# Optimization experiments

Hardware: AMD Instinct MI355X
Metric: run time of the kernel (lower is better)

Reference implementation:

```python
import jax, jax.numpy as jnp
import numpy as np

C_IN = 1024
N_HEADS = 16
C_HEAD = C_IN // N_HEADS  # 64
ROPE_BASE = 10000.0


def setup_inputs() -> dict:
    key = jax.random.key(0)
    ks = jax.random.split(key, 7)
    B, S = 2, 2048
    q = jax.random.normal(ks[0], (B, S, C_IN), dtype=jnp.float32)
    k = jax.random.normal(ks[1], (B, S, C_IN), dtype=jnp.float32)
    v = jax.random.normal(ks[2], (B, S, C_IN), dtype=jnp.float32)
    # nn.Linear weights [out, in], y = x @ W.T (no bias)
    sc = 1.0 / np.sqrt(C_IN)
    Wq = jax.random.uniform(ks[3], (C_IN, C_IN), jnp.float32, -sc, sc)
    Wk = jax.random.uniform(ks[4], (C_IN, C_IN), jnp.float32, -sc, sc)
    Wv = jax.random.uniform(ks[5], (C_IN, C_IN), jnp.float32, -sc, sc)
    Wo = jax.random.uniform(ks[6], (C_IN, C_IN), jnp.float32, -sc, sc)
    return {"q": q, "k": k, "v": v, "Wq": Wq, "Wk": Wk, "Wv": Wv, "Wo": Wo}


def _rope_tables(S, dtype):
    inv_freq = 1.0 / (ROPE_BASE ** (jnp.arange(0, C_HEAD, 2, dtype=jnp.float32) / C_HEAD))
    t = jnp.arange(S, dtype=jnp.float32)
    freqs = jnp.einsum('i,j->ij', t, inv_freq)          # [S, C_HEAD/2]
    emb = jnp.concatenate([freqs, freqs], axis=-1)      # [S, C_HEAD]
    cos = jnp.cos(emb)[None, None, :, :].astype(dtype)  # [1,1,S,D]
    sin = jnp.sin(emb)[None, None, :, :].astype(dtype)
    return cos, sin


def _rotate_half(x):
    x1, x2 = jnp.split(x, 2, axis=-1)
    return jnp.concatenate([-x2, x1], axis=-1)


def reference(q, k, v, Wq, Wk, Wv, Wo):
    B, S, _ = q.shape
    # QKV projections, reshape to [B, H, S, D]
    def proj(x, W):
        return (x @ W.T).reshape(B, -1, N_HEADS, C_HEAD).transpose(0, 2, 1, 3)
    qh, kh, vh = proj(q, Wq), proj(k, Wk), proj(v, Wv)
    # rotary embedding
    cos, sin = _rope_tables(S, qh.dtype)
    qh = qh * cos + _rotate_half(qh) * sin
    kh = kh * cos + _rotate_half(kh) * sin
    # scaled dot-product attention (no mask, dropout p=0)
    scale = 1.0 / np.sqrt(C_HEAD)
    scores = jnp.einsum('bhqd,bhkd->bhqk', qh, kh) * scale
    attn = jax.nn.softmax(scores, axis=-1)              # [B,H,S,S]
    out = jnp.einsum('bhqk,bhkd->bhqd', attn, vh)
    out = out.transpose(0, 2, 1, 3).reshape(B, S, N_HEADS * C_HEAD)
    out = out @ Wo.T
    return out, attn
```

## Files before the change

### kernel.cpp

```cpp
#include <hip/hip_runtime.h>
#include <cmath>

typedef __bf16 bhalf;
typedef __bf16 bf16x4 __attribute__((ext_vector_type(4)));
typedef __bf16 bf16x8 __attribute__((ext_vector_type(8)));
typedef float f32x4 __attribute__((ext_vector_type(4)));

#define MFMA16(a, b, c) __builtin_amdgcn_mfma_f32_16x16x32_bf16(a, b, c, 0, 0, 0)

namespace {
constexpr int Bn = 2, Sn = 2048, Cn = 1024, Hn = 16, Dn = 64;
constexpr int Zn = Bn * Hn;
constexpr int Mn = Bn * Sn;
}

__device__ __forceinline__ void cvt_hilo8(const float4& v0, const float4& v1,
                                          bf16x8& hi, bf16x8& lo) {
  float f[8] = {v0.x, v0.y, v0.z, v0.w, v1.x, v1.y, v1.z, v1.w};
#pragma unroll
  for (int i = 0; i < 8; ++i) {
    bhalf h = (bhalf)f[i];
    hi[i] = h;
    lo[i] = (bhalf)(f[i] - (float)h);
  }
}

template <int MODE, bool A_BF16>
__global__ __launch_bounds__(256) void proj_mfma(
    const void* __restrict__ Av, const void* __restrict__ AvLo,
    const float* __restrict__ W, float* __restrict__ out_f32,
    bhalf* __restrict__ dst_hi, bhalf* __restrict__ dst_lo) {
  __shared__ bhalf BsH[64][40];
  __shared__ bhalf BsL[64][40];
  const int tid = threadIdx.x;
  const int lane = tid & 63, w = tid >> 6;
  const int l15 = lane & 15, lg = lane >> 4;
  const int nB = blockIdx.x << 6, mB = blockIdx.y << 6;
  const int row = mB + w * 16 + l15;
  f32x4 acc[4] = {};

  const int sr = tid >> 2, sc = (tid & 3) << 3;
  for (int k0 = 0; k0 < Cn; k0 += 32) {
    {
      const float* wp = W + (size_t)(nB + sr) * Cn + k0 + sc;
      float4 w0 = *(const float4*)wp;
      float4 w1 = *(const float4*)(wp + 4);
      bf16x8 h, l;
      cvt_hilo8(w0, w1, h, l);
      *(bf16x8*)&BsH[sr][sc] = h;
      *(bf16x8*)&BsL[sr][sc] = l;
    }
    __syncthreads();
    bf16x8 aH, aL;
    if constexpr (A_BF16) {
      aH = *(const bf16x8*)((const bhalf*)Av + (size_t)row * Cn + k0 + lg * 8);
      aL = *(const bf16x8*)((const bhalf*)AvLo + (size_t)row * Cn + k0 + lg * 8);
    } else {
      const float* A = (const float*)Av;
      float4 a0 = *(const float4*)(A + (size_t)row * Cn + k0 + lg * 8);
      float4 a1 = *(const float4*)(A + (size_t)row * Cn + k0 + lg * 8 + 4);
      cvt_hilo8(a0, a1, aH, aL);
    }
#pragma unroll
    for (int j = 0; j < 4; ++j) {
      bf16x8 bH = *(const bf16x8*)&BsH[16 * j + l15][lg * 8];
      bf16x8 bL = *(const bf16x8*)&BsL[16 * j + l15][lg * 8];
      acc[j] = MFMA16(aH, bH, acc[j]);
      acc[j] = MFMA16(aH, bL, acc[j]);
      acc[j] = MFMA16(aL, bH, acc[j]);
    }
    __syncthreads();
  }

  const int mRow = mB + w * 16 + lg * 4;
  if constexpr (MODE == 0) {
#pragma unroll
    for (int j = 0; j < 4; ++j) {
      const int n = nB + 16 * j + l15;
#pragma unroll
      for (int r = 0; r < 4; ++r)
        out_f32[(size_t)(mRow + r) * Cn + n] = acc[j][r];
    }
  } else if constexpr (MODE == 1) {
    const int hh = nB >> 6;
#pragma unroll
    for (int jj = 0; jj < 2; ++jj) {
      const int d1 = 16 * jj + l15;
      const float invf = 1.0f / powf(10000.0f, (float)d1 * (1.0f / 32.0f));
#pragma unroll
      for (int r = 0; r < 4; ++r) {
        const int m = mRow + r;
        const int b = m >> 11, s = m & (Sn - 1);
        float sn, cs;
        sincosf((float)s * invf, &sn, &cs);
        const float y1 = acc[jj][r], y2 = acc[jj + 2][r];
        const float o1 = y1 * cs - y2 * sn;
        const float o2 = y2 * cs + y1 * sn;
        const size_t base = (((size_t)(b * Hn + hh)) * Sn + s) * Dn;
        bhalf h1 = (bhalf)o1, h2 = (bhalf)o2;
        dst_hi[base + d1] = h1;
        dst_lo[base + d1] = (bhalf)(o1 - (float)h1);
        dst_hi[base + d1 + 32] = h2;
        dst_lo[base + d1 + 32] = (bhalf)(o2 - (float)h2);
      }
    }
  } else {
    const int hh = nB >> 6;
#pragma unroll
    for (int j = 0; j < 4; ++j) {
      const int d = 16 * j + l15;
#pragma unroll
      for (int r = 0; r < 4; ++r) {
        const int m = mRow + r;
        const int b = m >> 11, s = m & (Sn - 1);
        dst_hi[(((size_t)(b * Hn + hh)) * Dn + d) * Sn + s] = (bhalf)acc[j][r];
      }
    }
  }
}

__device__ __forceinline__ void load_q(const bhalf* __restrict__ qhH,
                                       const bhalf* __restrict__ qhL,
                                       size_t zrow, int sBt, int l15, int lg,
                                       bf16x8 (&qH)[2][2], bf16x8 (&qL)[2][2]) {
#pragma unroll
  for (int qf = 0; qf < 2; ++qf)
#pragma unroll
    for (int sl = 0; sl < 2; ++sl) {
      const size_t off = (zrow + sBt + qf * 16 + l15) * Dn + sl * 32 + lg * 8;
      qH[qf][sl] = *(const bf16x8*)(qhH + off);
      qL[qf][sl] = *(const bf16x8*)(qhL + off);
    }
}

__global__ __launch_bounds__(256) void attn_fused(
    const bhalf* __restrict__ qhH, const bhalf* __restrict__ qhL,
    const bhalf* __restrict__ khH, const bhalf* __restrict__ khL,
    const bhalf* __restrict__ vt, float* __restrict__ attn,
    bhalf* __restrict__ ctxH, bhalf* __restrict__ ctxL) {
  __shared__ float pt[4][32][36];
  __shared__ float lsum[4][32];
  __shared__ float linv[32];

  const int tid = threadIdx.x, lane = tid & 63, w = tid >> 6;
  const int l15 = lane & 15, lg = lane >> 4;
  const int gx = blockIdx.x;
  const int z = gx & 31;
  const int gq = gx >> 5;
  const int sB0 = gq << 7;
  const int bb = z >> 4, hh = z & 15;
  const size_t zrow = (size_t)z * Sn;
  const size_t kRow = zrow * Dn;
  const int kw = w << 9;

  bf16x8 qHc[2][2], qLc[2][2], qHp[2][2], qLp[2][2];
  load_q(qhH, qhL, zrow, sB0, l15, lg, qHc, qLc);

  float invqB[2] = {0.f, 0.f};
  f32x4 acc[2][4];

#pragma unroll 1
  for (int tau = 0; tau <= 4; ++tau) {
    const bool hasA = (tau < 4), hasB = (tau > 0);
    const int sBb = sB0 + ((tau - 1) << 5);
    float sum0 = 0.f, sum1 = 0.f;
    if (hasB) {
#pragma unroll
      for (int qf = 0; qf < 2; ++qf)
#pragma unroll
        for (int g = 0; g < 4; ++g) acc[qf][g] = f32x4{0.f, 0.f, 0.f, 0.f};
    }

#pragma unroll 1
    for (int cc = 0; cc < 16; ++cc) {
      const int kbc = kw + (cc << 5);
#pragma unroll
      for (int t2 = 0; t2 < 2; ++t2) {
        const int kb = kbc + (t2 << 4);
        const bhalf* kp = khH + kRow + (size_t)(kb + l15) * Dn + lg * 8;
        const bhalf* kq = khL + kRow + (size_t)(kb + l15) * Dn + lg * 8;
        bf16x8 kH0 = *(const bf16x8*)kp, kH1 = *(const bf16x8*)(kp + 32);
        bf16x8 kL0 = *(const bf16x8*)kq, kL1 = *(const bf16x8*)(kq + 32);
        if (hasA) {
#pragma unroll
          for (int qf = 0; qf < 2; ++qf) {
            f32x4 cA = {}, cB = {};
            cA = MFMA16(kH0, qHc[qf][0], cA); cA = MFMA16(kH1, qHc[qf][1], cA);
            cB = MFMA16(kL0, qHc[qf][0], cB); cB = MFMA16(kL1, qHc[qf][1], cB);
            cA = MFMA16(kH0, qLc[qf][0], cA); cA = MFMA16(kH1, qLc[qf][1], cA);
            f32x4 c = cA + cB;
            float s = __expf(c[0] * 0.125f) + __expf(c[1] * 0.125f) +
                      __expf(c[2] * 0.125f) + __expf(c[3] * 0.125f);
            if (qf == 0) sum0 += s; else sum1 += s;
          }
        }
        if (hasB) {
#pragma unroll
          for (int qf = 0; qf < 2; ++qf) {
            f32x4 cA = {}, cB = {};
            cA = MFMA16(kH0, qHp[qf][0], cA); cA = MFMA16(kH1, qHp[qf][1], cA);
            cB = MFMA16(kL0, qHp[qf][0], cB); cB = MFMA16(kL1, qHp[qf][1], cB);
            cA = MFMA16(kH0, qLp[qf][0], cA); cA = MFMA16(kH1, qLp[qf][1], cA);
            f32x4 c = cA + cB;
            f32x4 p;
#pragma unroll
            for (int r = 0; r < 4; ++r)
              p[r] = __expf(c[r] * 0.125f) * invqB[qf];
            *(f32x4*)&pt[w][qf * 16 + l15][(t2 << 4) + (lg << 2)] = p;
          }
        }
      }
      if (hasB) {
        const int srow = lane >> 3, scol = (lane & 7) << 2;
#pragma unroll
        for (int s = 0; s < 4; ++s) {
          const int row = (s << 3) + srow;
          f32x4 vv = *(const f32x4*)&pt[w][row][scol];
          __builtin_nontemporal_store(
              vv, (f32x4*)(attn + (zrow + sBb + row) * Sn + kbc + scol));
        }
#pragma unroll
        for (int qf = 0; qf < 2; ++qf) {
          f32x4 pa = *(const f32x4*)&pt[w][qf * 16 + l15][lg << 3];
          f32x4 pc = *(const f32x4*)&pt[w][qf * 16 + l15][(lg << 3) + 4];
          bf16x8 pbv;
#pragma unroll
          for (int e = 0; e < 4; ++e) {
            pbv[e] = (bhalf)pa[e];
            pbv[4 + e] = (bhalf)pc[e];
          }
#pragma unroll
          for (int g = 0; g < 4; ++g) {
            const bf16x8 va = *(const bf16x8*)(
                vt + ((size_t)z * Dn + g * 16 + l15) * Sn + kbc + lg * 8);
            acc[qf][g] = MFMA16(va, pbv, acc[qf][g]);
          }
        }
      }
    }

    if (hasA) {
      sum0 += __shfl_xor(sum0, 16); sum0 += __shfl_xor(sum0, 32);
      sum1 += __shfl_xor(sum1, 16); sum1 += __shfl_xor(sum1, 32);
      if (lane < 16) {
        lsum[w][l15] = sum0;
        lsum[w][16 + l15] = sum1;
      }
    }
    __syncthreads();
    if (hasA && tid < 32)
      linv[tid] =
          1.0f / (lsum[0][tid] + lsum[1][tid] + lsum[2][tid] + lsum[3][tid]);
    if (hasB) {
      float* fb = (float*)&pt[w][0][0];
      float* fb0 = (float*)&pt[0][0][0];
      float* fb1 = (float*)&pt[1][0][0];
      float* fb2 = (float*)&pt[2][0][0];
      float* fb3 = (float*)&pt[3][0][0];
#pragma unroll
      for (int qf = 0; qf < 2; ++qf) {
#pragma unroll
        for (int g = 0; g < 4; ++g)
#pragma unroll
          for (int r = 0; r < 4; ++r)
            fb[l15 * 72 + g * 16 + lg * 4 + r] = acc[qf][g][r];
        __syncthreads();
        {
          const int qq = tid >> 4, d4 = (tid & 15) << 2;
          f32x4 rs = *(const f32x4*)&fb0[qq * 72 + d4];
          rs += *(const f32x4*)&fb1[qq * 72 + d4];
          rs += *(const f32x4*)&fb2[qq * 72 + d4];
          rs += *(const f32x4*)&fb3[qq * 72 + d4];
          const size_t off =
              ((size_t)bb * Sn + sBb + qf * 16 + qq) * Cn + hh * Dn + d4;
          bf16x4 hv, lv;
#pragma unroll
          for (int e = 0; e < 4; ++e) {
            bhalf h = (bhalf)rs[e];
            hv[e] = h;
            lv[e] = (bhalf)(rs[e] - (float)h);
          }
          *(bf16x4*)(ctxH + off) = hv;
          *(bf16x4*)(ctxL + off) = lv;
        }
        __syncthreads();
      }
    } else {
      __syncthreads();
    }
    if (hasA) {
      invqB[0] = linv[l15];
      invqB[1] = linv[16 + l15];
#pragma unroll
      for (int qf = 0; qf < 2; ++qf)
#pragma unroll
        for (int sl = 0; sl < 2; ++sl) {
          qHp[qf][sl] = qHc[qf][sl];
          qLp[qf][sl] = qLc[qf][sl];
        }
      if (tau < 3)
        load_q(qhH, qhL, zrow, sB0 + ((tau + 1) << 5), l15, lg, qHc, qLc);
    }
  }
}

extern "C" void kernel_launch(void* const* d_in, const int* in_sizes, int n_in,
                              void* d_out, int out_size, void* d_ws, size_t ws_size,
                              hipStream_t stream) {
  const float* q = (const float*)d_in[0];
  const float* k = (const float*)d_in[1];
  const float* v = (const float*)d_in[2];
  const float* Wq = (const float*)d_in[3];
  const float* Wk = (const float*)d_in[4];
  const float* Wv = (const float*)d_in[5];
  const float* Wo = (const float*)d_in[6];

  float* out = (float*)d_out;
  float* attn = out + (size_t)Mn * Cn;
  bhalf* vt = (bhalf*)d_out;

  bhalf* qhH = (bhalf*)d_ws;
  bhalf* qhL = qhH + (size_t)Mn * Cn;
  bhalf* khH = qhL + (size_t)Mn * Cn;
  bhalf* khL = khH + (size_t)Mn * Cn;
  bhalf* ctxH = khL + (size_t)Mn * Cn;
  bhalf* ctxL = ctxH + (size_t)Mn * Cn;

  dim3 gP(Cn / 64, Mn / 64);
  proj_mfma<1, false><<<gP, 256, 0, stream>>>(q, nullptr, Wq, nullptr, qhH, qhL);
  proj_mfma<1, false><<<gP, 256, 0, stream>>>(k, nullptr, Wk, nullptr, khH, khL);
  proj_mfma<2, false><<<gP, 256, 0, stream>>>(v, nullptr, Wv, nullptr, vt, nullptr);

  attn_fused<<<Zn * (Sn / 128), 256, 0, stream>>>(qhH, qhL, khH, khL, vt, attn,
                                                  ctxH, ctxL);

  proj_mfma<0, true><<<gP, 256, 0, stream>>>(ctxH, ctxL, Wo, out, nullptr, nullptr);
}
```

Baseline: 433.9 us.

## Double projection GEMM M-tile and split QK MFMA accumulator chains

```diff
diff --git a/kernel.cpp b/kernel.cpp
--- a/kernel.cpp
+++ b/kernel.cpp
@@ -35,9 +35,9 @@
   const int tid = threadIdx.x;
   const int lane = tid & 63, w = tid >> 6;
   const int l15 = lane & 15, lg = lane >> 4;
-  const int nB = blockIdx.x << 6, mB = blockIdx.y << 6;
-  const int row = mB + w * 16 + l15;
-  f32x4 acc[4] = {};
+  const int nB = blockIdx.x << 6, mB = blockIdx.y << 7;
+  const int row0 = mB + w * 32 + l15;
+  f32x4 acc[2][4] = {};
 
   const int sr = tid >> 2, sc = (tid & 3) << 3;
   for (int k0 = 0; k0 < Cn; k0 += 32) {
@@ -51,69 +51,79 @@
       *(bf16x8*)&BsL[sr][sc] = l;
     }
     __syncthreads();
-    bf16x8 aH, aL;
-    if constexpr (A_BF16) {
-      aH = *(const bf16x8*)((const bhalf*)Av + (size_t)row * Cn + k0 + lg * 8);
-      aL = *(const bf16x8*)((const bhalf*)AvLo + (size_t)row * Cn + k0 + lg * 8);
-    } else {
-      const float* A = (const float*)Av;
-      float4 a0 = *(const float4*)(A + (size_t)row * Cn + k0 + lg * 8);
-      float4 a1 = *(const float4*)(A + (size_t)row * Cn + k0 + lg * 8 + 4);
-      cvt_hilo8(a0, a1, aH, aL);
+    bf16x8 aH[2], aL[2];
+#pragma unroll
+    for (int rg = 0; rg < 2; ++rg) {
+      const size_t ro = (size_t)(row0 + rg * 16) * Cn + k0 + lg * 8;
+      if constexpr (A_BF16) {
+        aH[rg] = *(const bf16x8*)((const bhalf*)Av + ro);
+        aL[rg] = *(const bf16x8*)((const bhalf*)AvLo + ro);
+      } else {
+        const float* A = (const float*)Av;
+        float4 a0 = *(const float4*)(A + ro);
+        float4 a1 = *(const float4*)(A + ro + 4);
+        cvt_hilo8(a0, a1, aH[rg], aL[rg]);
+      }
     }
 #pragma unroll
     for (int j = 0; j < 4; ++j) {
       bf16x8 bH = *(const bf16x8*)&BsH[16 * j + l15][lg * 8];
       bf16x8 bL = *(const bf16x8*)&BsL[16 * j + l15][lg * 8];
-      acc[j] = MFMA16(aH, bH, acc[j]);
-      acc[j] = MFMA16(aH, bL, acc[j]);
-      acc[j] = MFMA16(aL, bH, acc[j]);
+#pragma unroll
+      for (int rg = 0; rg < 2; ++rg) {
+        acc[rg][j] = MFMA16(aH[rg], bH, acc[rg][j]);
+        acc[rg][j] = MFMA16(aH[rg], bL, acc[rg][j]);
+        acc[rg][j] = MFMA16(aL[rg], bH, acc[rg][j]);
+      }
     }
     __syncthreads();
   }
 
-  const int mRow = mB + w * 16 + lg * 4;
-  if constexpr (MODE == 0) {
-#pragma unroll
-    for (int j = 0; j < 4; ++j) {
-      const int n = nB + 16 * j + l15;
-#pragma unroll
-      for (int r = 0; r < 4; ++r)
-        out_f32[(size_t)(mRow + r) * Cn + n] = acc[j][r];
-    }
-  } else if constexpr (MODE == 1) {
-    const int hh = nB >> 6;
-#pragma unroll
-    for (int jj = 0; jj < 2; ++jj) {
-      const int d1 = 16 * jj + l15;
-      const float invf = 1.0f / powf(10000.0f, (float)d1 * (1.0f / 32.0f));
-#pragma unroll
-      for (int r = 0; r < 4; ++r) {
-        const int m = mRow + r;
-        const int b = m >> 11, s = m & (Sn - 1);
-        float sn, cs;
-        sincosf((float)s * invf, &sn, &cs);
-        const float y1 = acc[jj][r], y2 = acc[jj + 2][r];
-        const float o1 = y1 * cs - y2 * sn;
-        const float o2 = y2 * cs + y1 * sn;
-        const size_t base = (((size_t)(b * Hn + hh)) * Sn + s) * Dn;
-        bhalf h1 = (bhalf)o1, h2 = (bhalf)o2;
-        dst_hi[base + d1] = h1;
-        dst_lo[base + d1] = (bhalf)(o1 - (float)h1);
-        dst_hi[base + d1 + 32] = h2;
-        dst_lo[base + d1 + 32] = (bhalf)(o2 - (float)h2);
-      }
-    }
-  } else {
-    const int hh = nB >> 6;
-#pragma unroll
-    for (int j = 0; j < 4; ++j) {
-      const int d = 16 * j + l15;
-#pragma unroll
-      for (int r = 0; r < 4; ++r) {
-        const int m = mRow + r;
-        const int b = m >> 11, s = m & (Sn - 1);
-        dst_hi[(((size_t)(b * Hn + hh)) * Dn + d) * Sn + s] = (bhalf)acc[j][r];
+#pragma unroll
+  for (int rg = 0; rg < 2; ++rg) {
+    const int mRow = mB + w * 32 + rg * 16 + lg * 4;
+    if constexpr (MODE == 0) {
+#pragma unroll
+      for (int j = 0; j < 4; ++j) {
+        const int n = nB + 16 * j + l15;
+#pragma unroll
+        for (int r = 0; r < 4; ++r)
+          out_f32[(size_t)(mRow + r) * Cn + n] = acc[rg][j][r];
+      }
+    } else if constexpr (MODE == 1) {
+      const int hh = nB >> 6;
+#pragma unroll
+      for (int jj = 0; jj < 2; ++jj) {
+        const int d1 = 16 * jj + l15;
+        const float invf = 1.0f / powf(10000.0f, (float)d1 * (1.0f / 32.0f));
+#pragma unroll
+        for (int r = 0; r < 4; ++r) {
+          const int m = mRow + r;
+          const int b = m >> 11, s = m & (Sn - 1);
+          float sn, cs;
+          sincosf((float)s * invf, &sn, &cs);
+          const float y1 = acc[rg][jj][r], y2 = acc[rg][jj + 2][r];
+          const float o1 = y1 * cs - y2 * sn;
+          const float o2 = y2 * cs + y1 * sn;
+          const size_t base = (((size_t)(b * Hn + hh)) * Sn + s) * Dn;
+          bhalf h1 = (bhalf)o1, h2 = (bhalf)o2;
+          dst_hi[base + d1] = h1;
+          dst_lo[base + d1] = (bhalf)(o1 - (float)h1);
+          dst_hi[base + d1 + 32] = h2;
+          dst_lo[base + d1 + 32] = (bhalf)(o2 - (float)h2);
+        }
+      }
+    } else {
+      const int hh = nB >> 6;
+#pragma unroll
+      for (int j = 0; j < 4; ++j) {
+        const int d = 16 * j + l15;
+#pragma unroll
+        for (int r = 0; r < 4; ++r) {
+          const int m = mRow + r;
+          const int b = m >> 11, s = m & (Sn - 1);
+          dst_hi[(((size_t)(b * Hn + hh)) * Dn + d) * Sn + s] = (bhalf)acc[rg][j][r];
+        }
       }
     }
   }
@@ -184,11 +194,11 @@
         if (hasA) {
 #pragma unroll
           for (int qf = 0; qf < 2; ++qf) {
-            f32x4 cA = {}, cB = {};
+            f32x4 cA = {}, cB = {}, cC = {};
             cA = MFMA16(kH0, qHc[qf][0], cA); cA = MFMA16(kH1, qHc[qf][1], cA);
             cB = MFMA16(kL0, qHc[qf][0], cB); cB = MFMA16(kL1, qHc[qf][1], cB);
-            cA = MFMA16(kH0, qLc[qf][0], cA); cA = MFMA16(kH1, qLc[qf][1], cA);
-            f32x4 c = cA + cB;
+            cC = MFMA16(kH0, qLc[qf][0], cC); cC = MFMA16(kH1, qLc[qf][1], cC);
+            f32x4 c = (cA + cB) + cC;
             float s = __expf(c[0] * 0.125f) + __expf(c[1] * 0.125f) +
                       __expf(c[2] * 0.125f) + __expf(c[3] * 0.125f);
             if (qf == 0) sum0 += s; else sum1 += s;
@@ -197,11 +207,11 @@
         if (hasB) {
 #pragma unroll
           for (int qf = 0; qf < 2; ++qf) {
-            f32x4 cA = {}, cB = {};
+            f32x4 cA = {}, cB = {}, cC = {};
             cA = MFMA16(kH0, qHp[qf][0], cA); cA = MFMA16(kH1, qHp[qf][1], cA);
             cB = MFMA16(kL0, qHp[qf][0], cB); cB = MFMA16(kL1, qHp[qf][1], cB);
-            cA = MFMA16(kH0, qLp[qf][0], cA); cA = MFMA16(kH1, qLp[qf][1], cA);
-            f32x4 c = cA + cB;
+            cC = MFMA16(kH0, qLp[qf][0], cC); cC = MFMA16(kH1, qLp[qf][1], cC);
+            f32x4 c = (cA + cB) + cC;
             f32x4 p;
 #pragma unroll
             for (int r = 0; r < 4; ++r)
@@ -326,7 +336,7 @@
   bhalf* ctxH = khL + (size_t)Mn * Cn;
   bhalf* ctxL = ctxH + (size_t)Mn * Cn;
 
-  dim3 gP(Cn / 64, Mn / 64);
+  dim3 gP(Cn / 64, Mn / 128);
   proj_mfma<1, false><<<gP, 256, 0, stream>>>(q, nullptr, Wq, nullptr, qhH, qhL);
   proj_mfma<1, false><<<gP, 256, 0, stream>>>(k, nullptr, Wk, nullptr, khH, khL);
   proj_mfma<2, false><<<gP, 256, 0, stream>>>(v, nullptr, Wv, nullptr, vt, nullptr);
```

After: 456.5 us. +5.2%, slower.

## Split attention block into compute and store warps with double-buffered P tiles

Applied to the files above, without the earlier changes.

```diff
diff --git a/kernel.cpp b/kernel.cpp
--- a/kernel.cpp
+++ b/kernel.cpp
@@ -133,17 +133,20 @@
     }
 }
 
-__global__ __launch_bounds__(256) void attn_fused(
+__global__ __launch_bounds__(512, 4) void attn_fused(
     const bhalf* __restrict__ qhH, const bhalf* __restrict__ qhL,
     const bhalf* __restrict__ khH, const bhalf* __restrict__ khL,
     const bhalf* __restrict__ vt, float* __restrict__ attn,
     bhalf* __restrict__ ctxH, bhalf* __restrict__ ctxL) {
-  __shared__ float pt[4][32][36];
+  __shared__ float ptd[2][4][32][36];
+  __shared__ float obuf[4][16][72];
   __shared__ float lsum[4][32];
   __shared__ float linv[32];
 
   const int tid = threadIdx.x, lane = tid & 63, w = tid >> 6;
   const int l15 = lane & 15, lg = lane >> 4;
+  const bool isC = (w < 4);
+  const int cw = w & 3;
   const int gx = blockIdx.x;
   const int z = gx & 31;
   const int gq = gx >> 5;
@@ -151,10 +154,10 @@
   const int bb = z >> 4, hh = z & 15;
   const size_t zrow = (size_t)z * Sn;
   const size_t kRow = zrow * Dn;
-  const int kw = w << 9;
+  const int kw = cw << 9;
 
   bf16x8 qHc[2][2], qLc[2][2], qHp[2][2], qLp[2][2];
-  load_q(qhH, qhL, zrow, sB0, l15, lg, qHc, qLc);
+  if (isC) load_q(qhH, qhL, zrow, sB0, l15, lg, qHc, qLc);
 
   float invqB[2] = {0.f, 0.f};
   f32x4 acc[2][4];
@@ -164,7 +167,7 @@
     const bool hasA = (tau < 4), hasB = (tau > 0);
     const int sBb = sB0 + ((tau - 1) << 5);
     float sum0 = 0.f, sum1 = 0.f;
-    if (hasB) {
+    if (hasB && isC) {
 #pragma unroll
       for (int qf = 0; qf < 2; ++qf)
 #pragma unroll
@@ -174,77 +177,83 @@
 #pragma unroll 1
     for (int cc = 0; cc < 16; ++cc) {
       const int kbc = kw + (cc << 5);
-#pragma unroll
-      for (int t2 = 0; t2 < 2; ++t2) {
-        const int kb = kbc + (t2 << 4);
-        const bhalf* kp = khH + kRow + (size_t)(kb + l15) * Dn + lg * 8;
-        const bhalf* kq = khL + kRow + (size_t)(kb + l15) * Dn + lg * 8;
-        bf16x8 kH0 = *(const bf16x8*)kp, kH1 = *(const bf16x8*)(kp + 32);
-        bf16x8 kL0 = *(const bf16x8*)kq, kL1 = *(const bf16x8*)(kq + 32);
-        if (hasA) {
+      if (isC) {
+#pragma unroll
+        for (int t2 = 0; t2 < 2; ++t2) {
+          const int kb = kbc + (t2 << 4);
+          const bhalf* kp = khH + kRow + (size_t)(kb + l15) * Dn + lg * 8;
+          const bhalf* kq = khL + kRow + (size_t)(kb + l15) * Dn + lg * 8;
+          bf16x8 kH0 = *(const bf16x8*)kp, kH1 = *(const bf16x8*)(kp + 32);
+          bf16x8 kL0 = *(const bf16x8*)kq, kL1 = *(const bf16x8*)(kq + 32);
+          if (hasA) {
+#pragma unroll
+            for (int qf = 0; qf < 2; ++qf) {
+              f32x4 cA = {}, cB = {};
+              cA = MFMA16(kH0, qHc[qf][0], cA); cA = MFMA16(kH1, qHc[qf][1], cA);
+              cB = MFMA16(kL0, qHc[qf][0], cB); cB = MFMA16(kL1, qHc[qf][1], cB);
+              cA = MFMA16(kH0, qLc[qf][0], cA); cA = MFMA16(kH1, qLc[qf][1], cA);
+              f32x4 c = cA + cB;
+              float s = __expf(c[0] * 0.125f) + __expf(c[1] * 0.125f) +
+                        __expf(c[2] * 0.125f) + __expf(c[3] * 0.125f);
+              if (qf == 0) sum0 += s; else sum1 += s;
+            }
+          }
+          if (hasB) {
+#pragma unroll
+            for (int qf = 0; qf < 2; ++qf) {
+              f32x4 cA = {}, cB = {};
+              cA = MFMA16(kH0, qHp[qf][0], cA); cA = MFMA16(kH1, qHp[qf][1], cA);
+              cB = MFMA16(kL0, qHp[qf][0], cB); cB = MFMA16(kL1, qHp[qf][1], cB);
+              cA = MFMA16(kH0, qLp[qf][0], cA); cA = MFMA16(kH1, qLp[qf][1], cA);
+              f32x4 c = cA + cB;
+              f32x4 p;
+#pragma unroll
+              for (int r = 0; r < 4; ++r)
+                p[r] = __expf(c[r] * 0.125f) * invqB[qf];
+              *(f32x4*)&ptd[cc & 1][cw][qf * 16 + l15][(t2 << 4) + (lg << 2)] = p;
+            }
+          }
+        }
+        if (hasB) {
 #pragma unroll
           for (int qf = 0; qf < 2; ++qf) {
-            f32x4 cA = {}, cB = {};
-            cA = MFMA16(kH0, qHc[qf][0], cA); cA = MFMA16(kH1, qHc[qf][1], cA);
-            cB = MFMA16(kL0, qHc[qf][0], cB); cB = MFMA16(kL1, qHc[qf][1], cB);
-            cA = MFMA16(kH0, qLc[qf][0], cA); cA = MFMA16(kH1, qLc[qf][1], cA);
-            f32x4 c = cA + cB;
-            float s = __expf(c[0] * 0.125f) + __expf(c[1] * 0.125f) +
-                      __expf(c[2] * 0.125f) + __expf(c[3] * 0.125f);
-            if (qf == 0) sum0 += s; else sum1 += s;
-          }
-        }
-        if (hasB) {
-#pragma unroll
-          for (int qf = 0; qf < 2; ++qf) {
-            f32x4 cA = {}, cB = {};
-            cA = MFMA16(kH0, qHp[qf][0], cA); cA = MFMA16(kH1, qHp[qf][1], cA);
-            cB = MFMA16(kL0, qHp[qf][0], cB); cB = MFMA16(kL1, qHp[qf][1], cB);
-            cA = MFMA16(kH0, qLp[qf][0], cA); cA = MFMA16(kH1, qLp[qf][1], cA);
-            f32x4 c = cA + cB;
-            f32x4 p;
-#pragma unroll
-            for (int r = 0; r < 4; ++r)
-              p[r] = __expf(c[r] * 0.125f) * invqB[qf];
-            *(f32x4*)&pt[w][qf * 16 + l15][(t2 << 4) + (lg << 2)] = p;
-          }
-        }
-      }
-      if (hasB) {
+            f32x4 pa = *(const f32x4*)&ptd[cc & 1][cw][qf * 16 + l15][lg << 3];
+            f32x4 pc = *(const f32x4*)&ptd[cc & 1][cw][qf * 16 + l15][(lg << 3) + 4];
+            bf16x8 pbv;
+#pragma unroll
+            for (int e = 0; e < 4; ++e) {
+              pbv[e] = (bhalf)pa[e];
+              pbv[4 + e] = (bhalf)pc[e];
+            }
+#pragma unroll
+            for (int g = 0; g < 4; ++g) {
+              const bf16x8 va = *(const bf16x8*)(
+                  vt + ((size_t)z * Dn + g * 16 + l15) * Sn + kbc + lg * 8);
+              acc[qf][g] = MFMA16(va, pbv, acc[qf][g]);
+            }
+          }
+        }
+      } else if (hasB && cc > 0) {
+        const int dc = cc - 1;
+        const int kbd = kw + (dc << 5);
         const int srow = lane >> 3, scol = (lane & 7) << 2;
 #pragma unroll
         for (int s = 0; s < 4; ++s) {
           const int row = (s << 3) + srow;
-          f32x4 vv = *(const f32x4*)&pt[w][row][scol];
+          f32x4 vv = *(const f32x4*)&ptd[dc & 1][cw][row][scol];
           __builtin_nontemporal_store(
-              vv, (f32x4*)(attn + (zrow + sBb + row) * Sn + kbc + scol));
-        }
-#pragma unroll
-        for (int qf = 0; qf < 2; ++qf) {
-          f32x4 pa = *(const f32x4*)&pt[w][qf * 16 + l15][lg << 3];
-          f32x4 pc = *(const f32x4*)&pt[w][qf * 16 + l15][(lg << 3) + 4];
-          bf16x8 pbv;
-#pragma unroll
-          for (int e = 0; e < 4; ++e) {
-            pbv[e] = (bhalf)pa[e];
-            pbv[4 + e] = (bhalf)pc[e];
-          }
-#pragma unroll
-          for (int g = 0; g < 4; ++g) {
-            const bf16x8 va = *(const bf16x8*)(
-                vt + ((size_t)z * Dn + g * 16 + l15) * Sn + kbc + lg * 8);
-            acc[qf][g] = MFMA16(va, pbv, acc[qf][g]);
-          }
-        }
-      }
-    }
-
-    if (hasA) {
+              vv, (f32x4*)(attn + (zrow + sBb + row) * Sn + kbd + scol));
+        }
+      }
+      __syncthreads();
+    }
+
+    if (hasA && isC) {
       sum0 += __shfl_xor(sum0, 16); sum0 += __shfl_xor(sum0, 32);
       sum1 += __shfl_xor(sum1, 16); sum1 += __shfl_xor(sum1, 32);
       if (lane < 16) {
-        lsum[w][l15] = sum0;
-        lsum[w][16 + l15] = sum1;
+        lsum[cw][l15] = sum0;
+        lsum[cw][16 + l15] = sum1;
       }
     }
     __syncthreads();
@@ -252,25 +261,32 @@
       linv[tid] =
           1.0f / (lsum[0][tid] + lsum[1][tid] + lsum[2][tid] + lsum[3][tid]);
     if (hasB) {
-      float* fb = (float*)&pt[w][0][0];
-      float* fb0 = (float*)&pt[0][0][0];
-      float* fb1 = (float*)&pt[1][0][0];
-      float* fb2 = (float*)&pt[2][0][0];
-      float* fb3 = (float*)&pt[3][0][0];
 #pragma unroll
       for (int qf = 0; qf < 2; ++qf) {
-#pragma unroll
-        for (int g = 0; g < 4; ++g)
-#pragma unroll
-          for (int r = 0; r < 4; ++r)
-            fb[l15 * 72 + g * 16 + lg * 4 + r] = acc[qf][g][r];
+        if (isC) {
+#pragma unroll
+          for (int g = 0; g < 4; ++g)
+#pragma unroll
+            for (int r = 0; r < 4; ++r)
+              obuf[cw][l15][g * 16 + lg * 4 + r] = acc[qf][g][r];
+        } else if (qf == 0) {
+          const int kbd = kw + (15 << 5);
+          const int srow = lane >> 3, scol = (lane & 7) << 2;
+#pragma unroll
+          for (int s = 0; s < 4; ++s) {
+            const int row = (s << 3) + srow;
+            f32x4 vv = *(const f32x4*)&ptd[1][cw][row][scol];
+            __builtin_nontemporal_store(
+                vv, (f32x4*)(attn + (zrow + sBb + row) * Sn + kbd + scol));
+          }
+        }
         __syncthreads();
-        {
+        if (tid < 256) {
           const int qq = tid >> 4, d4 = (tid & 15) << 2;
-          f32x4 rs = *(const f32x4*)&fb0[qq * 72 + d4];
-          rs += *(const f32x4*)&fb1[qq * 72 + d4];
-          rs += *(const f32x4*)&fb2[qq * 72 + d4];
-          rs += *(const f32x4*)&fb3[qq * 72 + d4];
+          f32x4 rs = *(const f32x4*)&obuf[0][qq][d4];
+          rs += *(const f32x4*)&obuf[1][qq][d4];
+          rs += *(const f32x4*)&obuf[2][qq][d4];
+          rs += *(const f32x4*)&obuf[3][qq][d4];
           const size_t off =
               ((size_t)bb * Sn + sBb + qf * 16 + qq) * Cn + hh * Dn + d4;
           bf16x4 hv, lv;
@@ -288,7 +304,7 @@
     } else {
       __syncthreads();
     }
-    if (hasA) {
+    if (hasA && isC) {
       invqB[0] = linv[l15];
       invqB[1] = linv[16 + l15];
 #pragma unroll
@@ -331,7 +347,7 @@
   proj_mfma<1, false><<<gP, 256, 0, stream>>>(k, nullptr, Wk, nullptr, khH, khL);
   proj_mfma<2, false><<<gP, 256, 0, stream>>>(v, nullptr, Wv, nullptr, vt, nullptr);
 
-  attn_fused<<<Zn * (Sn / 128), 256, 0, stream>>>(qhH, qhL, khH, khL, vt, attn,
+  attn_fused<<<Zn * (Sn / 128), 512, 0, stream>>>(qhH, qhL, khH, khL, vt, attn,
                                                   ctxH, ctxL);
 
   proj_mfma<0, true><<<gP, 256, 0, stream>>>(ctxH, ctxL, Wo, out, nullptr, nullptr);
```

New measurement: 728.3 us. +67.8%, slower.
